# Optimization experiments

Hardware: AMD Instinct MI355X
Metric: run time of the kernel (lower is better)

The kernel has to match this reference:

```python
import jax, jax.numpy as jnp
import numpy as np

HIDDEN = 1024
STATE = 16
DT_RANK = 64


def setup_inputs() -> dict:
    key = jax.random.key(0)
    ks = jax.random.split(key, 5)
    B, S = 2, 2048
    x = jax.random.normal(ks[0], (B, S, HIDDEN), dtype=jnp.float32)
    # lecun_normal-ish init scales
    W_xproj = jax.random.normal(ks[1], (HIDDEN, STATE * 2 + DT_RANK), dtype=jnp.float32) / np.sqrt(HIDDEN)
    W_dt = jax.random.normal(ks[2], (DT_RANK, HIDDEN), dtype=jnp.float32) / np.sqrt(DT_RANK)
    b_dt = jnp.zeros((HIDDEN,), dtype=jnp.float32)
    A_log = jax.random.normal(ks[3], (STATE, HIDDEN), dtype=jnp.float32) / np.sqrt(STATE)
    return {"x": x, "W_xproj": W_xproj, "W_dt": W_dt, "b_dt": b_dt, "A_log": A_log}


def reference(x, W_xproj, W_dt, b_dt, A_log):
    # x: [B, S, D]
    xp = x @ W_xproj                       # [B, S, 2N + R]
    Bm = xp[..., :STATE]                    # [B, S, N]
    Cm = xp[..., STATE:2 * STATE]           # [B, S, N]
    dt = jax.nn.softplus(xp[..., 2 * STATE:] @ W_dt + b_dt)  # [B, S, D]
    A = -jnp.exp(A_log)                     # [N, D]
    A_bar = jnp.exp(A[None, None] * dt[:, :, None, :])        # [B, S, N, D]
    Bu = Bm[:, :, :, None] * dt[:, :, None, :] * x[:, :, None, :]  # [B, S, N, D]

    def scan_fn(h, inp):
        A_t, Bu_t = inp
        h = A_t * h + Bu_t
        return h, h

    h0 = jnp.zeros(Bu.shape[:1] + Bu.shape[2:], dtype=x.dtype)   # [B, N, D]
    _, h_all = jax.lax.scan(scan_fn, h0,
                            (A_bar.transpose(1, 0, 2, 3), Bu.transpose(1, 0, 2, 3)))  # [S, B, N, D]
    y = jnp.einsum('bsn,sbnd->bsd', Cm, h_all)  # [B, S, D]
    return y
```

## Files before the change

kernel.cpp:

```cpp
#include <hip/hip_runtime.h>
#include <math.h>

#define HIDDEN 1024
#define NSTATE 16
#define DTRANK 64
#define BB 2
#define SS 2048
#define ROWS (BB*SS)
#define XPC 96
#define CH 64
#define CL 32
#define BND (BB*NSTATE*HIDDEN)
#define LOG2E 1.44269504088896f

#define RT 64
#define KSPL 8

__global__ __launch_bounds__(256) void k_xproj2(const float* __restrict__ x,
                                                const float* __restrict__ W,
                                                float* __restrict__ part) {
    __shared__ float xs[RT * 32];
    __shared__ float wt[96 * 36];
    int t  = threadIdx.x;
    int rt = blockIdx.x >> 3;
    int ks = blockIdx.x & 7;
    int r0 = rt * RT;
    int k0 = ks * 128;
    int cg = t & 15, rg = t >> 4;

    float acc[4][6];
    #pragma unroll
    for (int a = 0; a < 4; ++a)
        #pragma unroll
        for (int b = 0; b < 6; ++b) acc[a][b] = 0.f;

    for (int ch = 0; ch < 4; ++ch) {
        int kc = k0 + ch * 32;
        __syncthreads();
        #pragma unroll
        for (int m = 0; m < 2; ++m) {
            int e = t + m * 256;
            int row = e >> 3, kb = e & 7;
            float4 v = *(const float4*)&x[(r0 + row) * HIDDEN + kc + kb * 4];
            int kbp = kb ^ ((row >> 2) & 7);
            *(float4*)&xs[row * 32 + kbp * 4] = v;
        }
        #pragma unroll
        for (int m = 0; m < 3; ++m) {
            int f = t + m * 256;
            int kr = f / 24, cq = f % 24;
            float4 v = *(const float4*)&W[(kc + kr) * XPC + cq * 4];
            wt[(cq * 4 + 0) * 36 + kr] = v.x;
            wt[(cq * 4 + 1) * 36 + kr] = v.y;
            wt[(cq * 4 + 2) * 36 + kr] = v.z;
            wt[(cq * 4 + 3) * 36 + kr] = v.w;
        }
        __syncthreads();
        #pragma unroll
        for (int kg = 0; kg < 8; ++kg) {
            float4 wv[6], xv[4];
            #pragma unroll
            for (int j = 0; j < 6; ++j)
                wv[j] = *(float4*)&wt[(cg + 16 * j) * 36 + kg * 4];
            #pragma unroll
            for (int rr = 0; rr < 4; ++rr) {
                int row = rg * 4 + rr;
                xv[rr] = *(float4*)&xs[row * 32 + ((kg ^ ((row >> 2) & 7)) * 4)];
            }
            #pragma unroll
            for (int rr = 0; rr < 4; ++rr)
                #pragma unroll
                for (int j = 0; j < 6; ++j) {
                    acc[rr][j] = fmaf(xv[rr].x, wv[j].x, acc[rr][j]);
                    acc[rr][j] = fmaf(xv[rr].y, wv[j].y, acc[rr][j]);
                    acc[rr][j] = fmaf(xv[rr].z, wv[j].z, acc[rr][j]);
                    acc[rr][j] = fmaf(xv[rr].w, wv[j].w, acc[rr][j]);
                }
        }
    }
    #pragma unroll
    for (int rr = 0; rr < 4; ++rr)
        #pragma unroll
        for (int j = 0; j < 6; ++j)
            part[ks * (ROWS * XPC) + (r0 + rg * 4 + rr) * XPC + cg + 16 * j] = acc[rr][j];
}

__global__ void k_rdt(const float* __restrict__ part, const float* __restrict__ Wdt,
                      const float* __restrict__ bdt, float* __restrict__ xp,
                      float* __restrict__ dt) {
    __shared__ float xs[8 * 64];
    int t = threadIdx.x;
    int r0 = blockIdx.x * 8;
    #pragma unroll
    for (int m = 0; m < 3; ++m) {
        int o = t + m * 256;
        int row = o / 96, col = o % 96;
        float s = 0.f;
        #pragma unroll
        for (int p = 0; p < KSPL; ++p)
            s += part[p * (ROWS * XPC) + (r0 + row) * XPC + col];
        xp[(r0 + row) * XPC + col] = s;
        if (col >= 2 * NSTATE) xs[row * 64 + (col - 2 * NSTATE)] = s;
    }
    __syncthreads();
    float4 acc[8];
    float4 b = *(const float4*)&bdt[t * 4];
    #pragma unroll
    for (int rr = 0; rr < 8; ++rr) acc[rr] = b;
    #pragma unroll 4
    for (int k = 0; k < DTRANK; ++k) {
        float4 w = *(const float4*)&Wdt[k * HIDDEN + t * 4];
        #pragma unroll
        for (int rr = 0; rr < 8; ++rr) {
            float s = xs[rr * 64 + k];
            acc[rr].x = fmaf(s, w.x, acc[rr].x);
            acc[rr].y = fmaf(s, w.y, acc[rr].y);
            acc[rr].z = fmaf(s, w.z, acc[rr].z);
            acc[rr].w = fmaf(s, w.w, acc[rr].w);
        }
    }
    #pragma unroll
    for (int rr = 0; rr < 8; ++rr) {
        float4 a = acc[rr], o;
        o.x = fmaxf(a.x, 0.f) + log1pf(__expf(-fabsf(a.x)));
        o.y = fmaxf(a.y, 0.f) + log1pf(__expf(-fabsf(a.y)));
        o.z = fmaxf(a.z, 0.f) + log1pf(__expf(-fabsf(a.z)));
        o.w = fmaxf(a.w, 0.f) + log1pf(__expf(-fabsf(a.w)));
        *(float4*)&dt[(r0 + rr) * HIDDEN + t * 4] = o;
    }
}

__global__ __launch_bounds__(256, 4)
void k_pass1(const float* __restrict__ x, const float* __restrict__ dt,
             const float* __restrict__ xp, const float* __restrict__ Alog,
             float* __restrict__ P, float* __restrict__ Q) {
    int bid = blockIdx.x;
    int dblk = bid & 3;
    int b = (bid >> 2) & 1;
    int c = bid >> 3;
    int d = dblk * 256 + threadIdx.x;
    float A2[NSTATE], Pv[NSTATE], Qv[NSTATE];
    #pragma unroll
    for (int n = 0; n < NSTATE; ++n) {
        A2[n] = -__expf(Alog[n*HIDDEN + d]) * LOG2E;
        Pv[n] = 1.f; Qv[n] = 0.f;
    }
    int s0 = c * CL;
    for (int i = 0; i < CL; ++i) {
        int r = b*SS + s0 + i;
        float dv = dt[r*HIDDEN + d];
        float xv = x[r*HIDDEN + d];
        float bm[NSTATE];
        *(float4*)&bm[0]  = *(const float4*)&xp[r*XPC + 0];
        *(float4*)&bm[4]  = *(const float4*)&xp[r*XPC + 4];
        *(float4*)&bm[8]  = *(const float4*)&xp[r*XPC + 8];
        *(float4*)&bm[12] = *(const float4*)&xp[r*XPC + 12];
        float bx = dv * xv;
        #pragma unroll
        for (int n = 0; n < NSTATE; ++n) {
            float a = exp2f(A2[n] * dv);
            Qv[n] = fmaf(a, Qv[n], bm[n] * bx);
            Pv[n] *= a;
        }
    }
    int base = b*(NSTATE*HIDDEN) + d;
    #pragma unroll
    for (int n = 0; n < NSTATE; ++n) {
        P[c*BND + base + n*HIDDEN] = Pv[n];
        Q[c*BND + base + n*HIDDEN] = Qv[n];
    }
}

__global__ void k_pass2(float* __restrict__ P, const float* __restrict__ Q) {
    int bnd = blockIdx.x * 256 + threadIdx.x;
    float h = 0.f;
    for (int cb = 0; cb < CH / 8; ++cb) {
        float p[8], q[8];
        #pragma unroll
        for (int j = 0; j < 8; ++j) {
            int idx = (cb*8 + j)*BND + bnd;
            p[j] = P[idx]; q[j] = Q[idx];
        }
        #pragma unroll
        for (int j = 0; j < 8; ++j) {
            int idx = (cb*8 + j)*BND + bnd;
            P[idx] = h;
            h = fmaf(p[j], h, q[j]);
        }
    }
}

__global__ __launch_bounds__(256, 4)
void k_pass3(const float* __restrict__ x, const float* __restrict__ dt,
             const float* __restrict__ xp, const float* __restrict__ Alog,
             const float* __restrict__ Hs, float* __restrict__ y) {
    int bid = blockIdx.x;
    int dblk = bid & 3;
    int b = (bid >> 2) & 1;
    int c = bid >> 3;
    int d = dblk * 256 + threadIdx.x;

    float A2[NSTATE], h[NSTATE];
    #pragma unroll
    for (int n = 0; n < NSTATE; ++n) {
        A2[n] = -__expf(Alog[n*HIDDEN + d]) * LOG2E;
        h[n] = Hs[c*BND + b*(NSTATE*HIDDEN) + n*HIDDEN + d];
    }
    int s0 = c * CL;
    for (int i = 0; i < CL; ++i) {
        int r = b*SS + s0 + i;
        float dv = dt[r*HIDDEN + d];
        float xv = x[r*HIDDEN + d];
        float bx = dv * xv;
        float bm[NSTATE], cm[NSTATE];
        *(float4*)&bm[0]  = *(const float4*)&xp[r*XPC + 0];
        *(float4*)&bm[4]  = *(const float4*)&xp[r*XPC + 4];
        *(float4*)&bm[8]  = *(const float4*)&xp[r*XPC + 8];
        *(float4*)&bm[12] = *(const float4*)&xp[r*XPC + 12];
        *(float4*)&cm[0]  = *(const float4*)&xp[r*XPC + 16];
        *(float4*)&cm[4]  = *(const float4*)&xp[r*XPC + 20];
        *(float4*)&cm[8]  = *(const float4*)&xp[r*XPC + 24];
        *(float4*)&cm[12] = *(const float4*)&xp[r*XPC + 28];
        float yv = 0.f;
        #pragma unroll
        for (int n = 0; n < NSTATE; ++n) {
            float a = exp2f(A2[n] * dv);
            h[n] = fmaf(a, h[n], bm[n] * bx);
            yv = fmaf(cm[n], h[n], yv);
        }
        y[r*HIDDEN + d] = yv;
    }
}

extern "C" void kernel_launch(void* const* d_in, const int* in_sizes, int n_in,
                              void* d_out, int out_size, void* d_ws, size_t ws_size,
                              hipStream_t stream) {
    const float* x    = (const float*)d_in[0];
    const float* Wx   = (const float*)d_in[1];
    const float* Wdt  = (const float*)d_in[2];
    const float* bdt  = (const float*)d_in[3];
    const float* Alog = (const float*)d_in[4];
    float* y  = (float*)d_out;
    float* ws = (float*)d_ws;

    float* xp = ws;
    float* dt = xp + ROWS*XPC;
    float* A  = dt + ROWS*HIDDEN;
    float* part = A;
    float* P  = A;
    float* Q  = A + CH*BND;

    k_xproj2<<<(ROWS/RT)*KSPL, 256, 0, stream>>>(x, Wx, part);
    k_rdt<<<ROWS/8, 256, 0, stream>>>(part, Wdt, bdt, xp, dt);
    k_pass1<<<CH*BB*4, 256, 0, stream>>>(x, dt, xp, Alog, P, Q);
    k_pass2<<<BND/256, 256, 0, stream>>>(P, Q);
    k_pass3<<<CH*BB*4, 256, 0, stream>>>(x, dt, xp, Alog, P, y);
}
```

Before: 112.4 us.

## Fuse five kernels into one persistent kernel with global atomic barriers

Merges the x-projection GEMM, reduction/dt projection, chunk pass1, cross-chunk scan, and pass3 into a single 512-block kernel separated by software grid barriers on atomic counters. The aim is to remove four kernel launch gaps and their tail effects. The part buffer is moved to its own workspace region so it no longer aliases P/Q, and a memset is added to reset the barrier counters. This relies on all 512 blocks being co-resident, otherwise it deadlocks. It also lowers occupancy to 2 blocks per CU via launch bounds and leaves most blocks idle during the scan phase.

```diff
diff --git a/kernel.cpp b/kernel.cpp
--- a/kernel.cpp
+++ b/kernel.cpp
@@ -15,220 +15,237 @@
 
 #define RT 64
 #define KSPL 8
-
-__global__ __launch_bounds__(256) void k_xproj2(const float* __restrict__ x,
-                                                const float* __restrict__ W,
-                                                float* __restrict__ part) {
-    __shared__ float xs[RT * 32];
-    __shared__ float wt[96 * 36];
-    int t  = threadIdx.x;
-    int rt = blockIdx.x >> 3;
-    int ks = blockIdx.x & 7;
-    int r0 = rt * RT;
-    int k0 = ks * 128;
-    int cg = t & 15, rg = t >> 4;
-
-    float acc[4][6];
-    #pragma unroll
-    for (int a = 0; a < 4; ++a)
-        #pragma unroll
-        for (int b = 0; b < 6; ++b) acc[a][b] = 0.f;
-
-    for (int ch = 0; ch < 4; ++ch) {
-        int kc = k0 + ch * 32;
+#define NBLK 512
+
+__device__ __forceinline__ void gbar(int* c) {
+    __syncthreads();
+    if (threadIdx.x == 0) {
+        __threadfence();
+        atomicAdd(c, 1);
+        while (atomicAdd(c, 0) < NBLK)
+            __builtin_amdgcn_s_sleep(2);
+    }
+    __syncthreads();
+    __threadfence();
+}
+
+__global__ __launch_bounds__(256, 2)
+void k_fused(const float* __restrict__ x, const float* __restrict__ W,
+             const float* __restrict__ Wdt, const float* __restrict__ bdt,
+             const float* __restrict__ Alog,
+             float* __restrict__ part, float* __restrict__ xp,
+             float* __restrict__ dt, float* __restrict__ P,
+             float* __restrict__ Q, float* __restrict__ y,
+             int* __restrict__ bar) {
+    __shared__ float smem[96 * 36 + RT * 32];
+    float* wt = smem;
+    float* xs = smem + 96 * 36;
+
+    int t = threadIdx.x;
+    int bidx = blockIdx.x;
+
+    {
+        int rt = bidx >> 3;
+        int ks = bidx & 7;
+        int r0 = rt * RT;
+        int k0 = ks * 128;
+        int cg_ = t & 15, rg = t >> 4;
+
+        float acc[4][6];
+        #pragma unroll
+        for (int a = 0; a < 4; ++a)
+            #pragma unroll
+            for (int b = 0; b < 6; ++b) acc[a][b] = 0.f;
+
+        for (int ch = 0; ch < 4; ++ch) {
+            int kc = k0 + ch * 32;
+            __syncthreads();
+            #pragma unroll
+            for (int m = 0; m < 2; ++m) {
+                int e = t + m * 256;
+                int row = e >> 3, kb = e & 7;
+                float4 v = *(const float4*)&x[(r0 + row) * HIDDEN + kc + kb * 4];
+                int kbp = kb ^ ((row >> 2) & 7);
+                *(float4*)&xs[row * 32 + kbp * 4] = v;
+            }
+            #pragma unroll
+            for (int m = 0; m < 3; ++m) {
+                int f = t + m * 256;
+                int kr = f / 24, cq = f % 24;
+                float4 v = *(const float4*)&W[(kc + kr) * XPC + cq * 4];
+                wt[(cq * 4 + 0) * 36 + kr] = v.x;
+                wt[(cq * 4 + 1) * 36 + kr] = v.y;
+                wt[(cq * 4 + 2) * 36 + kr] = v.z;
+                wt[(cq * 4 + 3) * 36 + kr] = v.w;
+            }
+            __syncthreads();
+            #pragma unroll
+            for (int kg = 0; kg < 8; ++kg) {
+                float4 wv[6], xv[4];
+                #pragma unroll
+                for (int j = 0; j < 6; ++j)
+                    wv[j] = *(float4*)&wt[(cg_ + 16 * j) * 36 + kg * 4];
+                #pragma unroll
+                for (int rr = 0; rr < 4; ++rr) {
+                    int row = rg * 4 + rr;
+                    xv[rr] = *(float4*)&xs[row * 32 + ((kg ^ ((row >> 2) & 7)) * 4)];
+                }
+                #pragma unroll
+                for (int rr = 0; rr < 4; ++rr)
+                    #pragma unroll
+                    for (int j = 0; j < 6; ++j) {
+                        acc[rr][j] = fmaf(xv[rr].x, wv[j].x, acc[rr][j]);
+                        acc[rr][j] = fmaf(xv[rr].y, wv[j].y, acc[rr][j]);
+                        acc[rr][j] = fmaf(xv[rr].z, wv[j].z, acc[rr][j]);
+                        acc[rr][j] = fmaf(xv[rr].w, wv[j].w, acc[rr][j]);
+                    }
+            }
+        }
+        #pragma unroll
+        for (int rr = 0; rr < 4; ++rr)
+            #pragma unroll
+            for (int j = 0; j < 6; ++j)
+                part[ks * (ROWS * XPC) + (r0 + rg * 4 + rr) * XPC + cg_ + 16 * j] = acc[rr][j];
+    }
+    gbar(bar + 0);
+
+    {
+        float* xs2 = smem;
+        int r0 = bidx * 8;
+        #pragma unroll
+        for (int m = 0; m < 3; ++m) {
+            int o = t + m * 256;
+            int row = o / 96, col = o % 96;
+            float s = 0.f;
+            #pragma unroll
+            for (int p = 0; p < KSPL; ++p)
+                s += part[p * (ROWS * XPC) + (r0 + row) * XPC + col];
+            xp[(r0 + row) * XPC + col] = s;
+            if (col >= 2 * NSTATE) xs2[row * 64 + (col - 2 * NSTATE)] = s;
+        }
         __syncthreads();
-        #pragma unroll
-        for (int m = 0; m < 2; ++m) {
-            int e = t + m * 256;
-            int row = e >> 3, kb = e & 7;
-            float4 v = *(const float4*)&x[(r0 + row) * HIDDEN + kc + kb * 4];
-            int kbp = kb ^ ((row >> 2) & 7);
-            *(float4*)&xs[row * 32 + kbp * 4] = v;
-        }
-        #pragma unroll
-        for (int m = 0; m < 3; ++m) {
-            int f = t + m * 256;
-            int kr = f / 24, cq = f % 24;
-            float4 v = *(const float4*)&W[(kc + kr) * XPC + cq * 4];
-            wt[(cq * 4 + 0) * 36 + kr] = v.x;
-            wt[(cq * 4 + 1) * 36 + kr] = v.y;
-            wt[(cq * 4 + 2) * 36 + kr] = v.z;
-            wt[(cq * 4 + 3) * 36 + kr] = v.w;
-        }
-        __syncthreads();
-        #pragma unroll
-        for (int kg = 0; kg < 8; ++kg) {
-            float4 wv[6], xv[4];
-            #pragma unroll
-            for (int j = 0; j < 6; ++j)
-                wv[j] = *(float4*)&wt[(cg + 16 * j) * 36 + kg * 4];
-            #pragma unroll
-            for (int rr = 0; rr < 4; ++rr) {
-                int row = rg * 4 + rr;
-                xv[rr] = *(float4*)&xs[row * 32 + ((kg ^ ((row >> 2) & 7)) * 4)];
-            }
-            #pragma unroll
-            for (int rr = 0; rr < 4; ++rr)
-                #pragma unroll
-                for (int j = 0; j < 6; ++j) {
-                    acc[rr][j] = fmaf(xv[rr].x, wv[j].x, acc[rr][j]);
-                    acc[rr][j] = fmaf(xv[rr].y, wv[j].y, acc[rr][j]);
-                    acc[rr][j] = fmaf(xv[rr].z, wv[j].z, acc[rr][j]);
-                    acc[rr][j] = fmaf(xv[rr].w, wv[j].w, acc[rr][j]);
-                }
-        }
-    }
-    #pragma unroll
-    for (int rr = 0; rr < 4; ++rr)
-        #pragma unroll
-        for (int j = 0; j < 6; ++j)
-            part[ks * (ROWS * XPC) + (r0 + rg * 4 + rr) * XPC + cg + 16 * j] = acc[rr][j];
-}
-
-__global__ void k_rdt(const float* __restrict__ part, const float* __restrict__ Wdt,
-                      const float* __restrict__ bdt, float* __restrict__ xp,
-                      float* __restrict__ dt) {
-    __shared__ float xs[8 * 64];
-    int t = threadIdx.x;
-    int r0 = blockIdx.x * 8;
-    #pragma unroll
-    for (int m = 0; m < 3; ++m) {
-        int o = t + m * 256;
-        int row = o / 96, col = o % 96;
-        float s = 0.f;
-        #pragma unroll
-        for (int p = 0; p < KSPL; ++p)
-            s += part[p * (ROWS * XPC) + (r0 + row) * XPC + col];
-        xp[(r0 + row) * XPC + col] = s;
-        if (col >= 2 * NSTATE) xs[row * 64 + (col - 2 * NSTATE)] = s;
-    }
-    __syncthreads();
-    float4 acc[8];
-    float4 b = *(const float4*)&bdt[t * 4];
-    #pragma unroll
-    for (int rr = 0; rr < 8; ++rr) acc[rr] = b;
-    #pragma unroll 4
-    for (int k = 0; k < DTRANK; ++k) {
-        float4 w = *(const float4*)&Wdt[k * HIDDEN + t * 4];
+        float4 acc[8];
+        float4 b = *(const float4*)&bdt[t * 4];
+        #pragma unroll
+        for (int rr = 0; rr < 8; ++rr) acc[rr] = b;
+        #pragma unroll 4
+        for (int k = 0; k < DTRANK; ++k) {
+            float4 w = *(const float4*)&Wdt[k * HIDDEN + t * 4];
+            #pragma unroll
+            for (int rr = 0; rr < 8; ++rr) {
+                float s = xs2[rr * 64 + k];
+                acc[rr].x = fmaf(s, w.x, acc[rr].x);
+                acc[rr].y = fmaf(s, w.y, acc[rr].y);
+                acc[rr].z = fmaf(s, w.z, acc[rr].z);
+                acc[rr].w = fmaf(s, w.w, acc[rr].w);
+            }
+        }
         #pragma unroll
         for (int rr = 0; rr < 8; ++rr) {
-            float s = xs[rr * 64 + k];
-            acc[rr].x = fmaf(s, w.x, acc[rr].x);
-            acc[rr].y = fmaf(s, w.y, acc[rr].y);
-            acc[rr].z = fmaf(s, w.z, acc[rr].z);
-            acc[rr].w = fmaf(s, w.w, acc[rr].w);
-        }
-    }
-    #pragma unroll
-    for (int rr = 0; rr < 8; ++rr) {
-        float4 a = acc[rr], o;
-        o.x = fmaxf(a.x, 0.f) + log1pf(__expf(-fabsf(a.x)));
-        o.y = fmaxf(a.y, 0.f) + log1pf(__expf(-fabsf(a.y)));
-        o.z = fmaxf(a.z, 0.f) + log1pf(__expf(-fabsf(a.z)));
-        o.w = fmaxf(a.w, 0.f) + log1pf(__expf(-fabsf(a.w)));
-        *(float4*)&dt[(r0 + rr) * HIDDEN + t * 4] = o;
-    }
-}
-
-__global__ __launch_bounds__(256, 4)
-void k_pass1(const float* __restrict__ x, const float* __restrict__ dt,
-             const float* __restrict__ xp, const float* __restrict__ Alog,
-             float* __restrict__ P, float* __restrict__ Q) {
-    int bid = blockIdx.x;
-    int dblk = bid & 3;
-    int b = (bid >> 2) & 1;
-    int c = bid >> 3;
-    int d = dblk * 256 + threadIdx.x;
-    float A2[NSTATE], Pv[NSTATE], Qv[NSTATE];
-    #pragma unroll
-    for (int n = 0; n < NSTATE; ++n) {
-        A2[n] = -__expf(Alog[n*HIDDEN + d]) * LOG2E;
-        Pv[n] = 1.f; Qv[n] = 0.f;
-    }
-    int s0 = c * CL;
-    for (int i = 0; i < CL; ++i) {
-        int r = b*SS + s0 + i;
-        float dv = dt[r*HIDDEN + d];
-        float xv = x[r*HIDDEN + d];
-        float bm[NSTATE];
-        *(float4*)&bm[0]  = *(const float4*)&xp[r*XPC + 0];
-        *(float4*)&bm[4]  = *(const float4*)&xp[r*XPC + 4];
-        *(float4*)&bm[8]  = *(const float4*)&xp[r*XPC + 8];
-        *(float4*)&bm[12] = *(const float4*)&xp[r*XPC + 12];
-        float bx = dv * xv;
+            float4 a = acc[rr], o;
+            o.x = fmaxf(a.x, 0.f) + log1pf(__expf(-fabsf(a.x)));
+            o.y = fmaxf(a.y, 0.f) + log1pf(__expf(-fabsf(a.y)));
+            o.z = fmaxf(a.z, 0.f) + log1pf(__expf(-fabsf(a.z)));
+            o.w = fmaxf(a.w, 0.f) + log1pf(__expf(-fabsf(a.w)));
+            *(float4*)&dt[(r0 + rr) * HIDDEN + t * 4] = o;
+        }
+    }
+    gbar(bar + 1);
+
+    {
+        int dblk = bidx & 3;
+        int b = (bidx >> 2) & 1;
+        int c = bidx >> 3;
+        int d = dblk * 256 + t;
+        float A2[NSTATE], Pv[NSTATE], Qv[NSTATE];
         #pragma unroll
         for (int n = 0; n < NSTATE; ++n) {
-            float a = exp2f(A2[n] * dv);
-            Qv[n] = fmaf(a, Qv[n], bm[n] * bx);
-            Pv[n] *= a;
-        }
-    }
-    int base = b*(NSTATE*HIDDEN) + d;
-    #pragma unroll
-    for (int n = 0; n < NSTATE; ++n) {
-        P[c*BND + base + n*HIDDEN] = Pv[n];
-        Q[c*BND + base + n*HIDDEN] = Qv[n];
-    }
-}
-
-__global__ void k_pass2(float* __restrict__ P, const float* __restrict__ Q) {
-    int bnd = blockIdx.x * 256 + threadIdx.x;
-    float h = 0.f;
-    for (int cb = 0; cb < CH / 8; ++cb) {
-        float p[8], q[8];
-        #pragma unroll
-        for (int j = 0; j < 8; ++j) {
-            int idx = (cb*8 + j)*BND + bnd;
-            p[j] = P[idx]; q[j] = Q[idx];
-        }
-        #pragma unroll
-        for (int j = 0; j < 8; ++j) {
-            int idx = (cb*8 + j)*BND + bnd;
-            P[idx] = h;
-            h = fmaf(p[j], h, q[j]);
-        }
-    }
-}
-
-__global__ __launch_bounds__(256, 4)
-void k_pass3(const float* __restrict__ x, const float* __restrict__ dt,
-             const float* __restrict__ xp, const float* __restrict__ Alog,
-             const float* __restrict__ Hs, float* __restrict__ y) {
-    int bid = blockIdx.x;
-    int dblk = bid & 3;
-    int b = (bid >> 2) & 1;
-    int c = bid >> 3;
-    int d = dblk * 256 + threadIdx.x;
-
-    float A2[NSTATE], h[NSTATE];
-    #pragma unroll
-    for (int n = 0; n < NSTATE; ++n) {
-        A2[n] = -__expf(Alog[n*HIDDEN + d]) * LOG2E;
-        h[n] = Hs[c*BND + b*(NSTATE*HIDDEN) + n*HIDDEN + d];
-    }
-    int s0 = c * CL;
-    for (int i = 0; i < CL; ++i) {
-        int r = b*SS + s0 + i;
-        float dv = dt[r*HIDDEN + d];
-        float xv = x[r*HIDDEN + d];
-        float bx = dv * xv;
-        float bm[NSTATE], cm[NSTATE];
-        *(float4*)&bm[0]  = *(const float4*)&xp[r*XPC + 0];
-        *(float4*)&bm[4]  = *(const float4*)&xp[r*XPC + 4];
-        *(float4*)&bm[8]  = *(const float4*)&xp[r*XPC + 8];
-        *(float4*)&bm[12] = *(const float4*)&xp[r*XPC + 12];
-        *(float4*)&cm[0]  = *(const float4*)&xp[r*XPC + 16];
-        *(float4*)&cm[4]  = *(const float4*)&xp[r*XPC + 20];
-        *(float4*)&cm[8]  = *(const float4*)&xp[r*XPC + 24];
-        *(float4*)&cm[12] = *(const float4*)&xp[r*XPC + 28];
-        float yv = 0.f;
+            A2[n] = -__expf(Alog[n*HIDDEN + d]) * LOG2E;
+            Pv[n] = 1.f; Qv[n] = 0.f;
+        }
+        int s0 = c * CL;
+        for (int i = 0; i < CL; ++i) {
+            int r = b*SS + s0 + i;
+            float dv = dt[r*HIDDEN + d];
+            float xv = x[r*HIDDEN + d];
+            float bm[NSTATE];
+            *(float4*)&bm[0]  = *(const float4*)&xp[r*XPC + 0];
+            *(float4*)&bm[4]  = *(const float4*)&xp[r*XPC + 4];
+            *(float4*)&bm[8]  = *(const float4*)&xp[r*XPC + 8];
+            *(float4*)&bm[12] = *(const float4*)&xp[r*XPC + 12];
+            float bx = dv * xv;
+            #pragma unroll
+            for (int n = 0; n < NSTATE; ++n) {
+                float a = exp2f(A2[n] * dv);
+                Qv[n] = fmaf(a, Qv[n], bm[n] * bx);
+                Pv[n] *= a;
+            }
+        }
+        int base = b*(NSTATE*HIDDEN) + d;
         #pragma unroll
         for (int n = 0; n < NSTATE; ++n) {
-            float a = exp2f(A2[n] * dv);
-            h[n] = fmaf(a, h[n], bm[n] * bx);
-            yv = fmaf(cm[n], h[n], yv);
-        }
-        y[r*HIDDEN + d] = yv;
+            P[c*BND + base + n*HIDDEN] = Pv[n];
+            Q[c*BND + base + n*HIDDEN] = Qv[n];
+        }
+    }
+    gbar(bar + 2);
+
+    if (bidx < BND / 256) {
+        int bnd = bidx * 256 + t;
+        float h = 0.f;
+        for (int cb = 0; cb < CH / 8; ++cb) {
+            float p[8], q[8];
+            #pragma unroll
+            for (int j = 0; j < 8; ++j) {
+                int idx = (cb*8 + j)*BND + bnd;
+                p[j] = P[idx]; q[j] = Q[idx];
+            }
+            #pragma unroll
+            for (int j = 0; j < 8; ++j) {
+                int idx = (cb*8 + j)*BND + bnd;
+                P[idx] = h;
+                h = fmaf(p[j], h, q[j]);
+            }
+        }
+    }
+    gbar(bar + 3);
+
+    {
+        int dblk = bidx & 3;
+        int b = (bidx >> 2) & 1;
+        int c = bidx >> 3;
+        int d = dblk * 256 + t;
+
+        float A2[NSTATE], h[NSTATE];
+        #pragma unroll
+        for (int n = 0; n < NSTATE; ++n) {
+            A2[n] = -__expf(Alog[n*HIDDEN + d]) * LOG2E;
+            h[n] = P[c*BND + b*(NSTATE*HIDDEN) + n*HIDDEN + d];
+        }
+        int s0 = c * CL;
+        for (int i = 0; i < CL; ++i) {
+            int r = b*SS + s0 + i;
+            float dv = dt[r*HIDDEN + d];
+            float xv = x[r*HIDDEN + d];
+            float bx = dv * xv;
+            float bm[NSTATE], cm[NSTATE];
+            *(float4*)&bm[0]  = *(const float4*)&xp[r*XPC + 0];
+            *(float4*)&bm[4]  = *(const float4*)&xp[r*XPC + 4];
+            *(float4*)&bm[8]  = *(const float4*)&xp[r*XPC + 8];
+            *(float4*)&bm[12] = *(const float4*)&xp[r*XPC + 12];
+            *(float4*)&cm[0]  = *(const float4*)&xp[r*XPC + 16];
+            *(float4*)&cm[4]  = *(const float4*)&xp[r*XPC + 20];
+            *(float4*)&cm[8]  = *(const float4*)&xp[r*XPC + 24];
+            *(float4*)&cm[12] = *(const float4*)&xp[r*XPC + 28];
+            float yv = 0.f;
+            #pragma unroll
+            for (int n = 0; n < NSTATE; ++n) {
+                float a = exp2f(A2[n] * dv);
+                h[n] = fmaf(a, h[n], bm[n] * bx);
+                yv = fmaf(cm[n], h[n], yv);
+            }
+            y[r*HIDDEN + d] = yv;
+        }
     }
 }
 
@@ -243,16 +260,14 @@
     float* y  = (float*)d_out;
     float* ws = (float*)d_ws;
 
-    float* xp = ws;
-    float* dt = xp + ROWS*XPC;
-    float* A  = dt + ROWS*HIDDEN;
-    float* part = A;
-    float* P  = A;
-    float* Q  = A + CH*BND;
-
-    k_xproj2<<<(ROWS/RT)*KSPL, 256, 0, stream>>>(x, Wx, part);
-    k_rdt<<<ROWS/8, 256, 0, stream>>>(part, Wdt, bdt, xp, dt);
-    k_pass1<<<CH*BB*4, 256, 0, stream>>>(x, dt, xp, Alog, P, Q);
-    k_pass2<<<BND/256, 256, 0, stream>>>(P, Q);
-    k_pass3<<<CH*BB*4, 256, 0, stream>>>(x, dt, xp, Alog, P, y);
+    float* xp   = ws;
+    float* dt   = xp + ROWS*XPC;
+    float* part = dt + ROWS*HIDDEN;
+    float* P    = part + (size_t)KSPL*ROWS*XPC;
+    float* Q    = P + (size_t)CH*BND;
+    int*   bar  = (int*)(Q + (size_t)CH*BND);
+
+    hipMemsetAsync(bar, 0, 4 * sizeof(int), stream);
+    k_fused<<<NBLK, 256, 0, stream>>>(x, Wx, Wdt, bdt, Alog,
+                                      part, xp, dt, P, Q, y, bar);
 }
```

Result: slower. 405.6 us (+261.0%).
